# Performance work log

Measured on AMD Instinct MI355X. Metric: run time of the kernel, lower is better.

Reference implementation:

```python
import jax, jax.numpy as jnp
import numpy as np

D_MODEL = 1024
HEAD = 16
K_D = D_MODEL // HEAD
SEQ_LEN = 2048
BATCH = 4
NEG = 1e10


def setup_inputs() -> dict:
    key = jax.random.key(0)
    ks = jax.random.split(key, 5)
    x = jax.random.normal(ks[0], (BATCH, SEQ_LEN, D_MODEL), dtype=jnp.float32)
    # params (torch Linear stored as [out,in]; we store [in,out] and matmul directly)
    W_attn = jax.random.normal(ks[1], (D_MODEL, 3 * D_MODEL), dtype=jnp.float32) * 0.02
    b_attn = jnp.zeros((3 * D_MODEL,), dtype=jnp.float32)
    W_proj = jax.random.normal(ks[2], (D_MODEL, D_MODEL), dtype=jnp.float32) * 0.02
    b_proj = jnp.zeros((D_MODEL,), dtype=jnp.float32)
    return {"x": x, "W_attn": W_attn, "b_attn": b_attn, "W_proj": W_proj, "b_proj": b_proj}


def reference(x, W_attn, b_attn, W_proj, b_proj):
    B, S, D = x.shape
    qkv = x @ W_attn + b_attn                     # [B,S,3D]
    # NOTE: source splits as (value, query, key) in that order
    value, query, key = jnp.split(qkv, 3, axis=-1)

    def heads(t):  # [B,S,D] -> [B,H,S,k_d]
        return t.reshape(B, S, HEAD, K_D).transpose(0, 2, 1, 3)

    v, q, k = heads(value), heads(query), heads(key)
    present = jnp.stack((k, v))                   # [2,B,H,S,k_d]

    scores = jnp.einsum('bhqd,bhkd->bhqk', q, k) / jnp.sqrt(jnp.float32(K_D))
    bias = jnp.tril(jnp.ones((S, S), dtype=scores.dtype))[None, None]
    scores = scores * bias - NEG * (1.0 - bias)
    attn = jax.nn.softmax(scores, axis=-1)
    out = jnp.einsum('bhqk,bhkd->bhqd', attn, v)  # [B,H,S,k_d]
    out = out.transpose(0, 2, 1, 3).reshape(B, S, D)
    out = out @ W_proj + b_proj
    return out, present
```

## Files before the change

### kernel.cpp

```cpp
#include <hip/hip_runtime.h>

typedef __attribute__((ext_vector_type(8))) short short8;
typedef __attribute__((ext_vector_type(4))) short short4v;
typedef __attribute__((ext_vector_type(4))) float f32x4;
typedef __attribute__((ext_vector_type(16))) float f32x16;
typedef __attribute__((ext_vector_type(4))) unsigned int u32x4;
typedef __attribute__((ext_vector_type(2))) unsigned int u32x2;
typedef unsigned int u32;

#define D_MODEL 1024
#define HEADS 16
#define KD 64
#define SEQ 2048
#define BATCH 4
#define NTOK (BATCH*SEQ)
#define QKV_N (3*D_MODEL)

#define WAIT_VM(n) asm volatile("s_waitcnt vmcnt(" #n ")" ::: "memory")

__device__ inline float bf2f(unsigned short u) {
    unsigned x = ((unsigned)u) << 16;
    return __builtin_bit_cast(float, x);
}
__device__ inline unsigned short f2bf(float f) {
    unsigned u = __builtin_bit_cast(unsigned, f);
    u += 0x7FFFu + ((u >> 16) & 1u);
    return (unsigned short)(u >> 16);
}
__device__ __forceinline__ void gload_lds16(const unsigned short* g, unsigned short* l) {
    __builtin_amdgcn_global_load_lds(
        (const __attribute__((address_space(1))) void*)g,
        (__attribute__((address_space(3))) void*)l, 16, 0, 0);
}
__device__ __forceinline__ u32 cvtpk(float lo, float hi) {
    u32 r; asm("v_cvt_pk_bf16_f32 %0, %1, %2" : "=v"(r) : "v"(lo), "v"(hi)); return r;
}
__device__ __forceinline__ void pl32swap(u32& a, u32& b) {
#if __has_builtin(__builtin_amdgcn_permlane32_swap)
    u32x2 r = __builtin_amdgcn_permlane32_swap(a, b, 0, 0);
    a = r[0]; b = r[1];
#else
    u32 pa = (u32)__shfl_xor((int)a, 32, 64);
    u32 pb = (u32)__shfl_xor((int)b, 32, 64);
    bool hb = (threadIdx.x & 32) != 0;
    u32 na = hb ? pb : a;
    u32 nb = hb ? b : pa;
    a = na; b = nb;
#endif
}
__device__ __forceinline__ float pairmax(float x) {
    u32 a = __builtin_bit_cast(u32, x), b = a;
    pl32swap(a, b);
    return fmaxf(x, fmaxf(__builtin_bit_cast(float, a), __builtin_bit_cast(float, b)));
}
__device__ __forceinline__ float pairsum(float x) {
    u32 a = __builtin_bit_cast(u32, x), b = a;
    pl32swap(a, b);
    return __builtin_bit_cast(float, a) + __builtin_bit_cast(float, b);
}

__global__ __launch_bounds__(256) void cvt_kernel(
    const float* __restrict__ x, unsigned short* __restrict__ y)
{
    size_t i = (size_t)blockIdx.x * 256 + threadIdx.x;
    f32x4 a = *reinterpret_cast<const f32x4*>(x + i*8);
    f32x4 b = *reinterpret_cast<const f32x4*>(x + i*8 + 4);
    short8 o;
    #pragma unroll
    for (int j = 0; j < 4; ++j) { o[j] = (short)f2bf(a[j]); o[j+4] = (short)f2bf(b[j]); }
    *reinterpret_cast<short8*>(y + i*8) = o;
}

__global__ __launch_bounds__(256) void transpose_kernel(
    const float* __restrict__ W, unsigned short* __restrict__ WT, int K, int N)
{
    __shared__ unsigned short T[64][80];
    const int tid = threadIdx.x;
    const int n0 = blockIdx.x * 64, k0 = blockIdx.y * 64;

    int r  = tid >> 2;
    int cq = tid & 3;
    const float* src = W + (size_t)(k0 + r) * N + n0 + cq*16;
    #pragma unroll
    for (int q = 0; q < 4; ++q) {
        f32x4 v = *reinterpret_cast<const f32x4*>(src + q*4);
        #pragma unroll
        for (int j = 0; j < 4; ++j) T[cq*16 + q*4 + j][r] = f2bf(v[j]);
    }
    __syncthreads();
    int c  = tid >> 2;
    int rq = tid & 3;
    short8 o0 = *reinterpret_cast<const short8*>(&T[c][rq*16]);
    short8 o1 = *reinterpret_cast<const short8*>(&T[c][rq*16 + 8]);
    unsigned short* dst = WT + (size_t)(n0 + c) * K + k0 + rq*16;
    *reinterpret_cast<short8*>(dst)     = o0;
    *reinterpret_cast<short8*>(dst + 8) = o1;
}

template<int Y_F32, int FUSE>
__global__ __launch_bounds__(256) void gemm_bt_kernel(
    const unsigned short* __restrict__ A, const unsigned short* __restrict__ BT,
    const float* __restrict__ bias, void* __restrict__ Yv,
    unsigned short* __restrict__ vtg, float* __restrict__ pres,
    int M, int N, int K)
{
    __shared__ unsigned short sA[2][128*64];
    __shared__ unsigned short sB[2][128*64];

    const int tid = threadIdx.x, lane = tid & 63, w = tid >> 6;
    const int l15 = lane & 15, lg = lane >> 4;

    const int nwg = gridDim.x * gridDim.y;
    const int bid = blockIdx.y * gridDim.x + blockIdx.x;
    const int swz = (bid & 7) * (nwg >> 3) + (bid >> 3);
    const int n0 = (swz % gridDim.x) * 128;
    const int m0 = (swz / gridDim.x) * 128;

    const int wr = w >> 1, wc = w & 1;

    f32x4 acc[4][4];
    #pragma unroll
    for (int m = 0; m < 4; ++m)
        #pragma unroll
        for (int n = 0; n < 4; ++n) acc[m][n] = f32x4{0,0,0,0};

    const int ldrow = (lane >> 3);
    const int slot  = lane & 7;
    const int nkt = K >> 6;

    #pragma unroll
    for (int i = 0; i < 4; ++i) {
        int kb  = w*4 + i;
        int row = kb*8 + ldrow;
        int sc  = slot ^ (row & 7);
        gload_lds16(&A [(size_t)(m0 + row) * K + sc*8], &sA[0][kb*512]);
        gload_lds16(&BT[(size_t)(n0 + row) * K + sc*8], &sB[0][kb*512]);
    }
    #pragma unroll
    for (int i = 0; i < 4; ++i) {
        int kb  = w*4 + i;
        int row = kb*8 + ldrow;
        int sc  = slot ^ (row & 7);
        gload_lds16(&A [(size_t)(m0 + row) * K + 64 + sc*8], &sA[1][kb*512]);
        gload_lds16(&BT[(size_t)(n0 + row) * K + 64 + sc*8], &sB[1][kb*512]);
    }

    for (int kt = 0; kt < nkt; ++kt) {
        const int buf = kt & 1;

        if (kt == nkt - 1) { WAIT_VM(0); } else { WAIT_VM(8); }
        __builtin_amdgcn_sched_barrier(0);
        __builtin_amdgcn_s_barrier();

        #pragma unroll
        for (int kk = 0; kk < 2; ++kk) {
            short8 af[4], bfr[4];
            #pragma unroll
            for (int m = 0; m < 4; ++m) {
                int row = wr*64 + m*16 + l15;
                int ch  = (4*kk + lg) ^ (row & 7);
                af[m] = *reinterpret_cast<const short8*>(&sA[buf][row*64 + ch*8]);
            }
            #pragma unroll
            for (int n = 0; n < 4; ++n) {
                int row = wc*64 + n*16 + l15;
                int ch  = (4*kk + lg) ^ (row & 7);
                bfr[n] = *reinterpret_cast<const short8*>(&sB[buf][row*64 + ch*8]);
            }
            __builtin_amdgcn_s_setprio(1);
            #pragma unroll
            for (int m = 0; m < 4; ++m)
                #pragma unroll
                for (int n = 0; n < 4; ++n)
                    acc[m][n] = __builtin_amdgcn_mfma_f32_16x16x32_bf16(
                        af[m], bfr[n], acc[m][n], 0, 0, 0);
            __builtin_amdgcn_s_setprio(0);
        }

        __builtin_amdgcn_s_barrier();
        __builtin_amdgcn_sched_barrier(0);
        if (kt + 2 < nkt) {
            const int k2 = (kt + 2) << 6;
            #pragma unroll
            for (int i = 0; i < 4; ++i) {
                int kb  = w*4 + i;
                int row = kb*8 + ldrow;
                int sc  = slot ^ (row & 7);
                gload_lds16(&A [(size_t)(m0 + row) * K + k2 + sc*8], &sA[buf][kb*512]);
                gload_lds16(&BT[(size_t)(n0 + row) * K + k2 + sc*8], &sB[buf][kb*512]);
            }
        }
    }

    #pragma unroll
    for (int n = 0; n < 4; ++n) {
        int col = n0 + wc*64 + n*16 + l15;
        float bv = bias[col];
        #pragma unroll
        for (int m = 0; m < 4; ++m) {
            int row0 = m0 + wr*64 + m*16 + lg*4;
            float v0 = acc[m][n][0] + bv;
            float v1 = acc[m][n][1] + bv;
            float v2 = acc[m][n][2] + bv;
            float v3 = acc[m][n][3] + bv;
            if (Y_F32) {
                float* Y = (float*)Yv;
                Y[(size_t)(row0+0) * N + col] = v0;
                Y[(size_t)(row0+1) * N + col] = v1;
                Y[(size_t)(row0+2) * N + col] = v2;
                Y[(size_t)(row0+3) * N + col] = v3;
            } else {
                unsigned short* Y = (unsigned short*)Yv;
                Y[(size_t)(row0+0) * N + col] = f2bf(v0);
                Y[(size_t)(row0+1) * N + col] = f2bf(v1);
                Y[(size_t)(row0+2) * N + col] = f2bf(v2);
                Y[(size_t)(row0+3) * N + col] = f2bf(v3);
            }
            if (FUSE && n0 < D_MODEL) {
                int hh = col >> 6, dd = col & 63;
                int bb = row0 >> 11, ss = row0 & (SEQ - 1);
                short4v pk;
                pk[0] = (short)f2bf(v0); pk[1] = (short)f2bf(v1);
                pk[2] = (short)f2bf(v2); pk[3] = (short)f2bf(v3);
                *reinterpret_cast<short4v*>(
                    vtg + (((size_t)bb*HEADS + hh)*KD + dd)*SEQ + ss) = pk;
                float* pv = pres + (size_t)BATCH*HEADS*SEQ*KD
                          + (((size_t)bb*HEADS + hh)*SEQ + ss)*KD + dd;
                pv[0] = v0; pv[KD] = v1; pv[2*KD] = v2; pv[3*KD] = v3;
            }
            if (FUSE && n0 >= 2*D_MODEL) {
                int rel = col - 2*D_MODEL;
                int hh = rel >> 6, dd = rel & 63;
                int bb = row0 >> 11, ss = row0 & (SEQ - 1);
                float* pk2 = pres + (((size_t)bb*HEADS + hh)*SEQ + ss)*KD + dd;
                pk2[0] = v0; pk2[KD] = v1; pk2[2*KD] = v2; pk2[3*KD] = v3;
            }
        }
    }
}

__global__ __launch_bounds__(512) void attn_kernel(
    const unsigned short* __restrict__ qkv,
    const unsigned short* __restrict__ vtg,
    unsigned short* __restrict__ aout)
{
    __shared__ unsigned short Kl[2][64*64];
    __shared__ unsigned short Vl[2][64*64];

    const int tid  = threadIdx.x;
    const int lane = tid & 63;
    const int w    = tid >> 6;
    const int wg   = w >> 2;
    const int wl   = w & 3;
    const int l31  = lane & 31, hi = lane >> 5;

    const int bid = blockIdx.x;
    const int hb  = bid & 63;
    const int i   = 7 - (bid >> 6);
    const int qb  = 2*i + wg;
    const int h = hb & 15, b = hb >> 4;

    const unsigned short* base  = qkv + (size_t)b * SEQ * QKV_N;
    const unsigned short* vbase = vtg + ((size_t)b * HEADS + h) * KD * SEQ;
    const int qoff = D_MODEL + h*KD;
    const int koff = 2*D_MODEL + h*KD;

    const float SCALE2 = 0.125f * 1.44269504088896f;
    const float THR_RAW = 44.36f;

    const int ldrow = lane >> 3;
    const int slot  = lane & 7;
    const int ksw   = l31 & 7;

    const int q0 = qb * 128;
    const int qrow  = q0 + wl*32 + l31;
    const int qminw = q0 + wl*32;

    short8 qf[4];
    #pragma unroll
    for (int ks = 0; ks < 4; ++ks)
        qf[ks] = *reinterpret_cast<const short8*>(
            base + (size_t)qrow * QKV_N + qoff + ks*16 + hi*8);

    f32x16 o0, o1;
    #pragma unroll
    for (int r = 0; r < 16; ++r) { o0[r] = 0.f; o1[r] = 0.f; }
    float m = -1e30f, msc = -1e30f * 0.180336887f, sr = 0.f;

    const int nt = 4*i + 4;

    {
        int row = w*8 + ldrow, sc = slot ^ (row & 7);
        gload_lds16(&base[(size_t)row * QKV_N + koff + sc*8], &Kl[0][w*512]);
        gload_lds16(&vbase[(size_t)row * SEQ + sc*8],         &Vl[0][w*512]);
        gload_lds16(&base[(size_t)(64 + row) * QKV_N + koff + sc*8], &Kl[1][w*512]);
        gload_lds16(&vbase[(size_t)row * SEQ + 64 + sc*8],           &Vl[1][w*512]);
    }

    for (int t = 0; t < nt; ++t) {
        const int buf = t & 1;

        if (t == nt - 1) { WAIT_VM(0); } else { WAIT_VM(2); }
        __builtin_amdgcn_sched_barrier(0);
        __builtin_amdgcn_s_barrier();

        const int d0 = qminw - t*64;
        if (d0 > -32) {
            f32x16 sa, sb;
            #pragma unroll
            for (int r = 0; r < 16; ++r) { sa[r] = 0.f; sb[r] = 0.f; }
            __builtin_amdgcn_s_setprio(1);
            #pragma unroll
            for (int ks = 0; ks < 4; ++ks) {
                short8 kf = *reinterpret_cast<const short8*>(
                    &Kl[buf][l31*64 + ((2*ks + hi) ^ ksw)*8]);
                sa = __builtin_amdgcn_mfma_f32_32x32x16_bf16(kf, qf[ks], sa, 0, 0, 0);
            }
            #pragma unroll
            for (int ks = 0; ks < 4; ++ks) {
                short8 kf = *reinterpret_cast<const short8*>(
                    &Kl[buf][(32 + l31)*64 + ((2*ks + hi) ^ ksw)*8]);
                sb = __builtin_amdgcn_mfma_f32_32x32x16_bf16(kf, qf[ks], sb, 0, 0, 0);
            }
            __builtin_amdgcn_s_setprio(0);

            if (d0 <= 32) {
                const int kqA = l31 + d0      - 4*hi;
                const int kqB = l31 + d0 - 32 - 4*hi;
                #pragma unroll
                for (int r = 0; r < 16; ++r) {
                    const int cr = (r & 3) + 8*(r >> 2);
                    if (d0 == 0) sa[r] = (cr <= kqA) ? sa[r] : -1e30f;
                    sb[r] = (cr <= kqB) ? sb[r] : -1e30f;
                }
            }

            float x[8];
            #pragma unroll
            for (int ii = 0; ii < 8; ++ii)
                x[ii] = fmaxf(fmaxf(sa[2*ii], sa[2*ii+1]), fmaxf(sb[2*ii], sb[2*ii+1]));
            float pm = fmaxf(fmaxf(fmaxf(x[0], x[1]), fmaxf(x[2], x[3])),
                             fmaxf(fmaxf(x[4], x[5]), fmaxf(x[6], x[7])));
            pm = pairmax(pm);
            if (!__all(pm <= m + THR_RAW)) {
                float mn  = fmaxf(m, pm);
                float fac = exp2f((m - mn) * SCALE2);
                sr *= fac;
                #pragma unroll
                for (int r = 0; r < 16; ++r) { o0[r] *= fac; o1[r] *= fac; }
                m = mn; msc = m * SCALE2;
            }

            #pragma unroll
            for (int r = 0; r < 16; ++r) {
                sa[r] = exp2f(sa[r]*SCALE2 - msc);
                sb[r] = exp2f(sb[r]*SCALE2 - msc);
            }
            float u[8];
            #pragma unroll
            for (int ii = 0; ii < 8; ++ii)
                u[ii] = (sa[2*ii] + sa[2*ii+1]) + (sb[2*ii] + sb[2*ii+1]);
            float ts = ((u[0]+u[1]) + (u[2]+u[3])) + ((u[4]+u[5]) + (u[6]+u[7]));
            sr += pairsum(ts);

            u32 WA[8], WB[8];
            #pragma unroll
            for (int wi = 0; wi < 8; ++wi) {
                WA[wi] = cvtpk(sa[2*wi], sa[2*wi+1]);
                WB[wi] = cvtpk(sb[2*wi], sb[2*wi+1]);
            }

            #pragma unroll
            for (int h32 = 0; h32 < 2; ++h32) {
                #pragma unroll
                for (int ks = 0; ks < 2; ++ks) {
                    u32 W0 = h32 ? WB[4*ks+0] : WA[4*ks+0];
                    u32 W1 = h32 ? WB[4*ks+1] : WA[4*ks+1];
                    u32 W2 = h32 ? WB[4*ks+2] : WA[4*ks+2];
                    u32 W3 = h32 ? WB[4*ks+3] : WA[4*ks+3];
                    u32 s0 = hi ? W0 : W2;
                    u32 s1 = hi ? W1 : W3;
                    u32 r0 = (u32)__shfl_xor((int)s0, 32, 64);
                    u32 r1 = (u32)__shfl_xor((int)s1, 32, 64);
                    u32x4 wv;
                    wv[0] = hi ? r0 : W0;
                    wv[1] = hi ? r1 : W1;
                    wv[2] = hi ? W2 : r0;
                    wv[3] = hi ? W3 : r1;
                    short8 pfrag = __builtin_bit_cast(short8, wv);
                    __builtin_amdgcn_s_setprio(1);
                    #pragma unroll
                    for (int dt = 0; dt < 2; ++dt) {
                        short8 vf = *reinterpret_cast<const short8*>(
                            &Vl[buf][(dt*32 + l31)*64 + ((4*h32 + 2*ks + hi) ^ ksw)*8]);
                        if (dt == 0)
                            o0 = __builtin_amdgcn_mfma_f32_32x32x16_bf16(vf, pfrag, o0, 0, 0, 0);
                        else
                            o1 = __builtin_amdgcn_mfma_f32_32x32x16_bf16(vf, pfrag, o1, 0, 0, 0);
                    }
                    __builtin_amdgcn_s_setprio(0);
                }
            }
        }

        __builtin_amdgcn_s_barrier();
        __builtin_amdgcn_sched_barrier(0);
        if (t + 2 < nt) {
            int row = w*8 + ldrow, sc = slot ^ (row & 7);
            gload_lds16(&base[(size_t)((t+2)*64 + row) * QKV_N + koff + sc*8],
                        &Kl[buf][w*512]);
            gload_lds16(&vbase[(size_t)row * SEQ + (t+2)*64 + sc*8],
                        &Vl[buf][w*512]);
        }
    }

    const float inv = 1.0f / sr;
    unsigned short* orow = aout + ((size_t)b * SEQ + qrow) * D_MODEL + h*KD;
    #pragma unroll
    for (int dt = 0; dt < 2; ++dt) {
        #pragma unroll
        for (int g = 0; g < 4; ++g) {
            short4v pk;
            #pragma unroll
            for (int j = 0; j < 4; ++j) {
                float v = (dt == 0 ? o0[4*g + j] : o1[4*g + j]) * inv;
                pk[j] = (short)f2bf(v);
            }
            *reinterpret_cast<short4v*>(orow + dt*32 + 8*g + 4*hi) = pk;
        }
    }
}

extern "C" void kernel_launch(void* const* d_in, const int* in_sizes, int n_in,
                              void* d_out, int out_size, void* d_ws, size_t ws_size,
                              hipStream_t stream)
{
    const float* x      = (const float*)d_in[0];
    const float* W_attn = (const float*)d_in[1];
    const float* b_attn = (const float*)d_in[2];
    const float* W_proj = (const float*)d_in[3];
    const float* b_proj = (const float*)d_in[4];
    float* out = (float*)d_out;

    unsigned short* qkv  = (unsigned short*)d_ws;
    unsigned short* xbf  = qkv + (size_t)NTOK * QKV_N;
    unsigned short* aout = xbf;
    unsigned short* WT   = xbf + (size_t)NTOK * D_MODEL;
    unsigned short* WpT  = WT + (size_t)QKV_N * D_MODEL;
    unsigned short* vtg  = WpT + (size_t)D_MODEL * D_MODEL;
    float* pres = out + (size_t)NTOK * D_MODEL;

    cvt_kernel<<<(NTOK * D_MODEL / 8) / 256, 256, 0, stream>>>(x, xbf);
    dim3 gt1(QKV_N / 64, D_MODEL / 64);
    transpose_kernel<<<gt1, 256, 0, stream>>>(W_attn, WT, D_MODEL, QKV_N);
    dim3 gt2(D_MODEL / 64, D_MODEL / 64);
    transpose_kernel<<<gt2, 256, 0, stream>>>(W_proj, WpT, D_MODEL, D_MODEL);

    dim3 g1(QKV_N / 128, NTOK / 128);
    gemm_bt_kernel<0, 1><<<g1, 256, 0, stream>>>(xbf, WT, b_attn, qkv, vtg, pres,
                                                 NTOK, QKV_N, D_MODEL);

    attn_kernel<<<512, 512, 0, stream>>>(qkv, vtg, aout);

    dim3 g2(D_MODEL / 128, NTOK / 128);
    gemm_bt_kernel<1, 0><<<g2, 256, 0, stream>>>(aout, WpT, b_proj, out,
                                                 nullptr, nullptr,
                                                 NTOK, D_MODEL, D_MODEL);
}
```

Baseline: 200.7 us.

## Use 256x256-tile 512-thread GEMM kernel for the QKV projection

Adds a new GEMM kernel with 256x256 output tiles, 8 waves and 128 KB of dynamic LDS double-buffering, and uses it for the QKV projection with the fused present/V-transpose epilogue. The larger tile raises arithmetic intensity per LDS and global load and halves the number of workgroups. The grid becomes 12x32=384 blocks, roughly 1.5 waves on 256 CUs, so tail imbalance and register pressure (128 accumulator floats per lane) are risks. The output projection keeps the old 128-tile kernel without the fusion template.

```diff
diff --git a/kernel.cpp b/kernel.cpp
--- a/kernel.cpp
+++ b/kernel.cpp
@@ -98,10 +98,165 @@
 }
 
 template<int Y_F32, int FUSE>
+__global__ __launch_bounds__(512) void gemm256_kernel(
+    const unsigned short* __restrict__ A, const unsigned short* __restrict__ BT,
+    const float* __restrict__ bias, void* __restrict__ Yv,
+    unsigned short* __restrict__ vtg, float* __restrict__ pres,
+    int M, int N, int K)
+{
+    extern __shared__ unsigned short lds[];
+    unsigned short* sA = lds;
+    unsigned short* sB = lds + 32768;
+
+    const int tid = threadIdx.x, lane = tid & 63, w = tid >> 6;
+    const int l15 = lane & 15, lg = lane >> 4;
+
+    const int nwg = gridDim.x * gridDim.y;
+    const int bid = blockIdx.y * gridDim.x + blockIdx.x;
+    const int swz = (bid & 7) * (nwg >> 3) + (bid >> 3);
+    const int n0 = (swz % gridDim.x) * 256;
+    const int m0 = (swz / gridDim.x) * 256;
+
+    const int wm = w >> 2;
+    const int wn = w & 3;
+
+    f32x4 acc[8][4];
+    #pragma unroll
+    for (int m = 0; m < 8; ++m)
+        #pragma unroll
+        for (int n = 0; n < 4; ++n) acc[m][n] = f32x4{0,0,0,0};
+
+    const int nkt = K >> 6;
+
+    #pragma unroll
+    for (int d = 0; d < 2; ++d) {
+        const int k = d << 6;
+        #pragma unroll
+        for (int j = 0; j < 4; ++j) {
+            int cidx = j*512 + tid;
+            int row = cidx >> 3, c = cidx & 7;
+            int sc = c ^ (row & 7);
+            gload_lds16(&A[(size_t)(m0 + row) * K + k + sc*8], &sA[d*16384 + cidx*8]);
+        }
+        #pragma unroll
+        for (int j = 0; j < 4; ++j) {
+            int cidx = j*512 + tid;
+            int row = cidx >> 3, c = cidx & 7;
+            int sc = c ^ (row & 7);
+            gload_lds16(&BT[(size_t)(n0 + row) * K + k + sc*8], &sB[d*16384 + cidx*8]);
+        }
+    }
+
+    for (int kt = 0; kt < nkt; ++kt) {
+        const int buf = kt & 1;
+
+        if (kt == nkt - 1) { WAIT_VM(0); } else { WAIT_VM(8); }
+        __builtin_amdgcn_sched_barrier(0);
+        __builtin_amdgcn_s_barrier();
+
+        short8 bf[4];
+        #pragma unroll
+        for (int p = 0; p < 4; ++p) {
+            const int ksub = p >> 1, mh = p & 1;
+            if (mh == 0) {
+                #pragma unroll
+                for (int nf = 0; nf < 4; ++nf) {
+                    int row = wn*64 + nf*16 + l15;
+                    int ch  = (4*ksub + lg) ^ (row & 7);
+                    bf[nf] = *reinterpret_cast<const short8*>(
+                        &sB[buf*16384 + row*64 + ch*8]);
+                }
+            }
+            short8 af[4];
+            #pragma unroll
+            for (int i = 0; i < 4; ++i) {
+                int row = wm*128 + (mh*4 + i)*16 + l15;
+                int ch  = (4*ksub + lg) ^ (row & 7);
+                af[i] = *reinterpret_cast<const short8*>(
+                    &sA[buf*16384 + row*64 + ch*8]);
+            }
+            __builtin_amdgcn_s_setprio(1);
+            #pragma unroll
+            for (int i = 0; i < 4; ++i)
+                #pragma unroll
+                for (int nf = 0; nf < 4; ++nf)
+                    acc[mh*4 + i][nf] = __builtin_amdgcn_mfma_f32_16x16x32_bf16(
+                        af[i], bf[nf], acc[mh*4 + i][nf], 0, 0, 0);
+            __builtin_amdgcn_s_setprio(0);
+        }
+
+        __builtin_amdgcn_s_barrier();
+        __builtin_amdgcn_sched_barrier(0);
+        if (kt + 2 < nkt) {
+            const int k2 = (kt + 2) << 6;
+            #pragma unroll
+            for (int j = 0; j < 4; ++j) {
+                int cidx = j*512 + tid;
+                int row = cidx >> 3, c = cidx & 7;
+                int sc = c ^ (row & 7);
+                gload_lds16(&A[(size_t)(m0 + row) * K + k2 + sc*8], &sA[buf*16384 + cidx*8]);
+            }
+            #pragma unroll
+            for (int j = 0; j < 4; ++j) {
+                int cidx = j*512 + tid;
+                int row = cidx >> 3, c = cidx & 7;
+                int sc = c ^ (row & 7);
+                gload_lds16(&BT[(size_t)(n0 + row) * K + k2 + sc*8], &sB[buf*16384 + cidx*8]);
+            }
+        }
+    }
+
+    #pragma unroll
+    for (int nf = 0; nf < 4; ++nf) {
+        int col = n0 + wn*64 + nf*16 + l15;
+        float bv = bias[col];
+        #pragma unroll
+        for (int mf = 0; mf < 8; ++mf) {
+            int row0 = m0 + wm*128 + mf*16 + lg*4;
+            float v0 = acc[mf][nf][0] + bv;
+            float v1 = acc[mf][nf][1] + bv;
+            float v2 = acc[mf][nf][2] + bv;
+            float v3 = acc[mf][nf][3] + bv;
+            if (Y_F32) {
+                float* Y = (float*)Yv;
+                Y[(size_t)(row0+0) * N + col] = v0;
+                Y[(size_t)(row0+1) * N + col] = v1;
+                Y[(size_t)(row0+2) * N + col] = v2;
+                Y[(size_t)(row0+3) * N + col] = v3;
+            } else {
+                unsigned short* Y = (unsigned short*)Yv;
+                Y[(size_t)(row0+0) * N + col] = f2bf(v0);
+                Y[(size_t)(row0+1) * N + col] = f2bf(v1);
+                Y[(size_t)(row0+2) * N + col] = f2bf(v2);
+                Y[(size_t)(row0+3) * N + col] = f2bf(v3);
+            }
+            if (FUSE && n0 < D_MODEL) {
+                int hh = col >> 6, dd = col & 63;
+                int bb = row0 >> 11, ss = row0 & (SEQ - 1);
+                short4v pk;
+                pk[0] = (short)f2bf(v0); pk[1] = (short)f2bf(v1);
+                pk[2] = (short)f2bf(v2); pk[3] = (short)f2bf(v3);
+                *reinterpret_cast<short4v*>(
+                    vtg + (((size_t)bb*HEADS + hh)*KD + dd)*SEQ + ss) = pk;
+                float* pv = pres + (size_t)BATCH*HEADS*SEQ*KD
+                          + (((size_t)bb*HEADS + hh)*SEQ + ss)*KD + dd;
+                pv[0] = v0; pv[KD] = v1; pv[2*KD] = v2; pv[3*KD] = v3;
+            }
+            if (FUSE && n0 >= 2*D_MODEL) {
+                int rel = col - 2*D_MODEL;
+                int hh = rel >> 6, dd = rel & 63;
+                int bb = row0 >> 11, ss = row0 & (SEQ - 1);
+                float* pk2 = pres + (((size_t)bb*HEADS + hh)*SEQ + ss)*KD + dd;
+                pk2[0] = v0; pk2[KD] = v1; pk2[2*KD] = v2; pk2[3*KD] = v3;
+            }
+        }
+    }
+}
+
+template<int Y_F32>
 __global__ __launch_bounds__(256) void gemm_bt_kernel(
     const unsigned short* __restrict__ A, const unsigned short* __restrict__ BT,
     const float* __restrict__ bias, void* __restrict__ Yv,
-    unsigned short* __restrict__ vtg, float* __restrict__ pres,
     int M, int N, int K)
 {
     __shared__ unsigned short sA[2][128*64];
@@ -215,25 +370,6 @@
                 Y[(size_t)(row0+1) * N + col] = f2bf(v1);
                 Y[(size_t)(row0+2) * N + col] = f2bf(v2);
                 Y[(size_t)(row0+3) * N + col] = f2bf(v3);
-            }
-            if (FUSE && n0 < D_MODEL) {
-                int hh = col >> 6, dd = col & 63;
-                int bb = row0 >> 11, ss = row0 & (SEQ - 1);
-                short4v pk;
-                pk[0] = (short)f2bf(v0); pk[1] = (short)f2bf(v1);
-                pk[2] = (short)f2bf(v2); pk[3] = (short)f2bf(v3);
-                *reinterpret_cast<short4v*>(
-                    vtg + (((size_t)bb*HEADS + hh)*KD + dd)*SEQ + ss) = pk;
-                float* pv = pres + (size_t)BATCH*HEADS*SEQ*KD
-                          + (((size_t)bb*HEADS + hh)*SEQ + ss)*KD + dd;
-                pv[0] = v0; pv[KD] = v1; pv[2*KD] = v2; pv[3*KD] = v3;
-            }
-            if (FUSE && n0 >= 2*D_MODEL) {
-                int rel = col - 2*D_MODEL;
-                int hh = rel >> 6, dd = rel & 63;
-                int bb = row0 >> 11, ss = row0 & (SEQ - 1);
-                float* pk2 = pres + (((size_t)bb*HEADS + hh)*SEQ + ss)*KD + dd;
-                pk2[0] = v0; pk2[KD] = v1; pk2[2*KD] = v2; pk2[3*KD] = v3;
             }
         }
     }
@@ -450,20 +586,23 @@
     unsigned short* vtg  = WpT + (size_t)D_MODEL * D_MODEL;
     float* pres = out + (size_t)NTOK * D_MODEL;
 
+    (void)hipFuncSetAttribute((const void*)gemm256_kernel<0, 1>,
+                              hipFuncAttributeMaxDynamicSharedMemorySize, 131072);
+
     cvt_kernel<<<(NTOK * D_MODEL / 8) / 256, 256, 0, stream>>>(x, xbf);
     dim3 gt1(QKV_N / 64, D_MODEL / 64);
     transpose_kernel<<<gt1, 256, 0, stream>>>(W_attn, WT, D_MODEL, QKV_N);
     dim3 gt2(D_MODEL / 64, D_MODEL / 64);
     transpose_kernel<<<gt2, 256, 0, stream>>>(W_proj, WpT, D_MODEL, D_MODEL);
 
-    dim3 g1(QKV_N / 128, NTOK / 128);
-    gemm_bt_kernel<0, 1><<<g1, 256, 0, stream>>>(xbf, WT, b_attn, qkv, vtg, pres,
-                                                 NTOK, QKV_N, D_MODEL);
+    dim3 g1(QKV_N / 256, NTOK / 256);
+    gemm256_kernel<0, 1><<<g1, 512, 131072, stream>>>(xbf, WT, b_attn, qkv,
+                                                      vtg, pres,
+                                                      NTOK, QKV_N, D_MODEL);
 
     attn_kernel<<<512, 512, 0, stream>>>(qkv, vtg, aout);
 
     dim3 g2(D_MODEL / 128, NTOK / 128);
-    gemm_bt_kernel<1, 0><<<g2, 256, 0, stream>>>(aout, WpT, b_proj, out,
-                                                 nullptr, nullptr,
-                                                 NTOK, D_MODEL, D_MODEL);
-}
+    gemm_bt_kernel<1><<<g2, 256, 0, stream>>>(aout, WpT, b_proj, out,
+                                              NTOK, D_MODEL, D_MODEL);
+}
```

Result: no change. 203.4 us (+1.4%).
